# Kernel tuning notes

Hardware: AMD Instinct MI355X
Metric: run time of the kernel (lower is better)

Reference implementation:

```python
import jax, jax.numpy as jnp
import numpy as np

B, S, D, H, E, KW = 2, 2048, 1024, 8, 128, 16  # batch, seq, d_model, heads, head_width, kernel_width


def setup_inputs() -> dict:
    key = jax.random.key(0)
    ks = jax.random.split(key, 10)
    sc = D ** -0.5
    x = jax.random.normal(ks[0], (B, S, D), dtype=jnp.float32)
    Wq = jax.random.normal(ks[1], (H, D, E), dtype=jnp.float32) * sc
    bq = jnp.zeros((H, E), dtype=jnp.float32)
    Wk = jax.random.normal(ks[2], (H, D, E), dtype=jnp.float32) * sc
    bk = jnp.zeros((H, E), dtype=jnp.float32)
    Wv = jax.random.normal(ks[3], (H, D, E), dtype=jnp.float32) * sc
    bv = jnp.zeros((H, E), dtype=jnp.float32)
    Wo = jax.random.normal(ks[4], (H, E, D), dtype=jnp.float32) * ((H * E) ** -0.5)
    bo = jnp.zeros((D,), dtype=jnp.float32)
    dilations = jnp.array([1, 1, 2, 2, 4, 4, 8, 8], dtype=jnp.int32)
    return {"x": x, "Wq": Wq, "bq": bq, "Wk": Wk, "bk": bk,
            "Wv": Wv, "bv": bv, "Wo": Wo, "bo": bo, "dilations": dilations}


def _windows(kh, vh, bkh, bvh, d):
    # kh, vh: [B, S, E] projected keys/values for one head; d: dilation (scalar int)
    s = kh.shape[1]
    # center-justified dilated window: positions i + d*j - d*(KW-1)//2
    pos = jnp.arange(s)[:, None] + d * jnp.arange(KW)[None, :] - (d * (KW - 1)) // 2
    valid = (pos >= 0) & (pos < s)            # [S, KW]
    posc = jnp.clip(pos, 0, s - 1)
    # padded positions hold the zero-embedding, whose projection is just the bias
    kw = jnp.where(valid[None, :, :, None], kh[:, posc, :], bkh)  # [B, S, KW, E]
    vw = jnp.where(valid[None, :, :, None], vh[:, posc, :], bvh)
    return kw, vw


def _lcsa(x, Wq, bq, Wk, bk, Wv, bv, Wo, bo, dilations):
    # per-head independent projections (Core.Linear with parallel shape [heads])
    q = jnp.einsum('bsd,hde->bhse', x, Wq) + bq[None, :, None, :]       # [B,H,S,E]
    k_all = jnp.einsum('bsd,hde->bhse', x, Wk) + bk[None, :, None, :]
    v_all = jnp.einsum('bsd,hde->bhse', x, Wv) + bv[None, :, None, :]
    # gather dilated local windows per head (project-then-gather; padded = bias)
    kw, vw = jax.vmap(_windows, in_axes=(1, 1, 0, 0, 0))(k_all, v_all, bk, bv, dilations)
    # kw, vw: [H, B, S, KW, E]
    logits = jnp.einsum('bhse,hbske->bhsk', q, kw)                       # [B,H,S,KW]
    score = jax.nn.softmax(logits, axis=-1)
    # NOTE: original divides by sqrt(d_head) AFTER softmax*value (faithful quirk)
    attn = jnp.einsum('bhsk,hbske->bhse', score, vw) / jnp.sqrt(jnp.asarray(E, x.dtype))
    out = jnp.einsum('bhse,hed->bsd', attn, Wo) + bo                     # dehead merge
    return out


def reference(x, Wq, bq, Wk, bk, Wv, bv, Wo, bo, dilations):
    return _lcsa(x, Wq, bq, Wk, bk, Wv, bv, Wo, bo, dilations)
```

## Files before the change

### kernel.cpp

```cpp
#include <hip/hip_runtime.h>
#include <stdint.h>

#define Bb 2
#define Ss 2048
#define Dd 1024
#define Hh 8
#define Ee 128
#define KWW 16
#define Mm (Bb*Ss)
#define Kk 1024

typedef unsigned short u16;
typedef __attribute__((ext_vector_type(8))) _Float16 f16x8;
typedef __attribute__((ext_vector_type(4))) float f32x4;

__device__ __forceinline__ u16 f2h(float f) {
  union { _Float16 h; u16 u; } v; v.h = (_Float16)f; return v.u;
}
__device__ __forceinline__ float h2f(u16 u) {
  union { u16 u; _Float16 h; } v; v.u = u; return (float)v.h;
}
__device__ __forceinline__ float h2f_lo(uint32_t w) { return h2f((u16)(w & 0xFFFF)); }
__device__ __forceinline__ float h2f_hi(uint32_t w) { return h2f((u16)(w >> 16)); }

__device__ __forceinline__ void gll16(const void* g, void* l) {
  __builtin_amdgcn_global_load_lds((const __attribute__((address_space(1))) void*)g,
                                   (__attribute__((address_space(3))) void*)l, 16, 0, 0);
}

__global__ __launch_bounds__(256) void prep(
    const float* __restrict__ x, const float* __restrict__ Wq,
    const float* __restrict__ Wk, const float* __restrict__ Wv,
    const float* __restrict__ Wo,
    u16* __restrict__ xh, u16* __restrict__ wT, u16* __restrict__ woT) {
  const int bid = blockIdx.x;
  const int tid = threadIdx.x;
  if (bid < 4096) {
    int i = (bid * 256 + tid) * 4;
    float4 f = *(const float4*)(x + i);
    uint64_t pk = (uint64_t)f2h(f.x) | ((uint64_t)f2h(f.y) << 16) |
                  ((uint64_t)f2h(f.z) << 32) | ((uint64_t)f2h(f.w) << 48);
    *(uint64_t*)(xh + i) = pk;
    return;
  }
  __shared__ float tile[32][33];
  const int tx = tid & 31, ty = tid >> 5;
  if (bid < 4096 + 3072) {
    const int idx = bid - 4096;
    const int z = idx >> 7, rem = idx & 127;
    const int h = z & 7;
    const float* W = (z < 8) ? Wq : (z < 16) ? Wk : Wv;
    const float* ib = W + (size_t)h * Dd * Ee;
    u16* ob = wT + (size_t)z * Ee * Kk;
    const int r0 = (rem & 31) * 32, c0 = (rem >> 5) * 32;
    #pragma unroll
    for (int kq = 0; kq < 4; kq++)
      tile[ty + 8*kq][tx] = ib[(size_t)(r0 + ty + 8*kq) * Ee + (c0 + tx)];
    __syncthreads();
    const int k = r0 + tx;
    #pragma unroll
    for (int kq = 0; kq < 4; kq++) {
      const int n = c0 + ty + 8*kq;
      ob[(((size_t)(k >> 3) * 128 + n) << 3) + (k & 7)] = f2h(tile[tx][ty + 8*kq]);
    }
  } else {
    const int idx = bid - (4096 + 3072);
    const int r0 = (idx & 31) * 32, c0 = (idx >> 5) * 32;
    const int C = Dd;
    #pragma unroll
    for (int kq = 0; kq < 4; kq++)
      tile[ty + 8*kq][tx] = Wo[(size_t)(r0 + ty + 8*kq) * C + (c0 + tx)];
    __syncthreads();
    const int k = r0 + tx;
    #pragma unroll
    for (int kq = 0; kq < 4; kq++) {
      const int n = c0 + ty + 8*kq;
      woT[(size_t)(n >> 7) * 131072 +
          (((size_t)(k >> 3) * 128 + (n & 127)) << 3) + (k & 7)] = f2h(tile[tx][ty + 8*kq]);
    }
  }
}

template<int MT>
__device__ __forceinline__ void gemm_core(
    const u16* __restrict__ A, const u16* __restrict__ Btf,
    u16* As, f32x4 (&acc)[MT / 32][4]) {
  constexpr int MI = MT / 32;
  const int tid = threadIdx.x;
  const int wave = tid >> 6;
  const int lane = tid & 63;
  const size_t lnoff = (size_t)(lane >> 3) * Kk + (size_t)(((lane & 7) ^ (lane >> 3)) * 8);

  const int wm = (wave >> 1) * (MT / 2);
  const int wn = (wave & 1) * 64;
  const int fr = lane & 15;
  const int q  = lane >> 4;
  const int sw = fr & 7;

  const u16* bptr = Btf + ((size_t)q * 128 + wn + fr) * 8;
  f16x8 bcur[8], bnxt[8];
  #pragma unroll
  for (int ks = 0; ks < 2; ks++)
    #pragma unroll
    for (int j = 0; j < 4; j++)
      bcur[ks * 4 + j] = *(const f16x8*)(bptr + (ks * 4) * 1024 + j * 128);

  #pragma unroll
  for (int i = 0; i < MI; i++)
    #pragma unroll
    for (int j = 0; j < 4; j++)
      #pragma unroll
      for (int r = 0; r < 4; r++) acc[i][j][r] = 0.0f;

  #pragma unroll
  for (int c = 0; c < MI; c++)
    gll16(A + lnoff + (size_t)((c * 4 + wave) * 8) * Kk, As + (c * 4 + wave) * 512);
  __syncthreads();

  for (int w = 0; w < Kk / 64; w++) {
    const int kt = w * 64;
    u16* cur = As + (w & 1) * (MT * 64);
    u16* nxt = As + ((w + 1) & 1) * (MT * 64);
    if (w + 1 < Kk / 64) {
      #pragma unroll
      for (int c = 0; c < MI; c++)
        gll16(A + lnoff + (size_t)((c * 4 + wave) * 8) * Kk + kt + 64, nxt + (c * 4 + wave) * 512);
    }
    const int ktn = (kt + 64) & (Kk - 1);
    #pragma unroll
    for (int ks = 0; ks < 2; ks++)
      #pragma unroll
      for (int j = 0; j < 4; j++)
        bnxt[ks * 4 + j] = *(const f16x8*)(bptr + ((ktn >> 3) + ks * 4) * 1024 + j * 128);
    #pragma unroll
    for (int ks = 0; ks < 2; ks++) {
      const int col = ((ks << 2) | q) ^ sw;
      f16x8 ah[MI];
      #pragma unroll
      for (int i = 0; i < MI; i++)
        ah[i] = *(const f16x8*)(cur + (wm + i * 16 + fr) * 64 + col * 8);
      #pragma unroll
      for (int i = 0; i < MI; i++)
        #pragma unroll
        for (int j = 0; j < 4; j++)
          acc[i][j] = __builtin_amdgcn_mfma_f32_16x16x32_f16(ah[i], bcur[ks * 4 + j], acc[i][j], 0, 0, 0);
    }
    __syncthreads();
    #pragma unroll
    for (int t = 0; t < 8; t++) bcur[t] = bnxt[t];
  }
}


__global__ __launch_bounds__(256) void gemm_qkv(
    const u16* __restrict__ xh, const u16* __restrict__ wT,
    const float* __restrict__ bq, const float* __restrict__ bk, const float* __restrict__ bv,
    u16* __restrict__ q, u16* __restrict__ k, u16* __restrict__ v) {
  __shared__ u16 As[128 * 64 * 2];
  const int m0 = blockIdx.x * 128;
  const int z = blockIdx.z;
  const int proj = z >> 3, h = z & 7;
  f32x4 acc[4][4];
  gemm_core<128>(xh + (size_t)m0 * Kk, wT + (size_t)z * (Ee * Kk), As, acc);

  u16* dst = proj == 0 ? q : (proj == 1 ? k : v);
  const float* bias = proj == 0 ? bq : (proj == 1 ? bk : bv);
  const int wave = threadIdx.x >> 6, lane = threadIdx.x & 63;
  const int wm = (wave >> 1) * 64, wn = (wave & 1) * 64;
  const int cn = lane & 15, rq4 = (lane >> 4) * 4;
  #pragma unroll
  for (int j = 0; j < 4; j++) {
    const int e = wn + j * 16 + cn;
    const float bb = bias[h * Ee + e];
    #pragma unroll
    for (int i = 0; i < 4; i++) {
      #pragma unroll
      for (int r = 0; r < 4; r++) {
        const int m = m0 + wm + i * 16 + rq4 + r;
        const int b = m >> 11, s = m & (Ss - 1);
        dst[(((size_t)(b * Hh + h)) * Ss + s) * Ee + e] = f2h(acc[i][j][r] + bb);
      }
    }
  }
}

__global__ __launch_bounds__(256) void gemm_out(
    const u16* __restrict__ attn, const u16* __restrict__ woT,
    const float* __restrict__ bo, float* __restrict__ out) {
  __shared__ u16 As[64 * 64 * 2];
  const int m0 = blockIdx.x * 64;
  const int n0 = blockIdx.y * 128;
  f32x4 acc[2][4];
  gemm_core<64>(attn + (size_t)m0 * Kk, woT + (size_t)blockIdx.y * 131072, As, acc);
  const int wave = threadIdx.x >> 6, lane = threadIdx.x & 63;
  const int wm = (wave >> 1) * 32, wn = (wave & 1) * 64;
  const int cn = lane & 15, rq4 = (lane >> 4) * 4;
  #pragma unroll
  for (int j = 0; j < 4; j++) {
    const int n = n0 + wn + j * 16 + cn;
    const float bb = bo[n];
    #pragma unroll
    for (int i = 0; i < 2; i++) {
      #pragma unroll
      for (int r = 0; r < 4; r++) {
        const int m = m0 + wm + i * 16 + rq4 + r;
        out[(size_t)m * Dd + n] = acc[i][j][r] + bb;
      }
    }
  }
}

__global__ __launch_bounds__(256) void attn_kernel(
    const u16* __restrict__ q, const u16* __restrict__ k, const u16* __restrict__ v,
    const float* __restrict__ bk, const float* __restrict__ bv,
    const int* __restrict__ dil, u16* __restrict__ attn) {
  const int nblk = (Bb * Hh * Ss) / 4;
  const int blk = (blockIdx.x & 7) * (nblk / 8) + (blockIdx.x >> 3);
  const int wid = blk * 4 + (threadIdx.x >> 6);
  const int lane = threadIdx.x & 63;
  const int s = wid & (Ss - 1);
  const int bh = wid >> 11;
  const int h = bh & 7, b = bh >> 3;
  const int d = dil[h];
  const size_t base = (size_t)bh * Ss * Ee;
  const u16* kp = k + base;
  const u16* vp = v + base;
  const uint32_t qw = *(const uint32_t*)(q + base + (size_t)s * Ee + 2 * lane);
  const float qx = h2f_lo(qw), qy = h2f_hi(qw);
  const float2 bk2 = ((const float2*)(bk + h * Ee))[lane];
  const float2 bv2 = ((const float2*)(bv + h * Ee))[lane];
  const int off = (d * (KWW - 1)) >> 1;
  const int J = (lane >> 2) & 15;

  float logit[KWW];
  #pragma unroll
  for (int j = 0; j < KWW; j++) {
    const int pos = s + d * j - off;
    if (pos >= 0 && pos < Ss) {
      uint32_t kw = *(const uint32_t*)(kp + (size_t)pos * Ee + 2 * lane);
      logit[j] = qx * h2f_lo(kw) + qy * h2f_hi(kw);
    } else {
      logit[j] = qx * bk2.x + qy * bk2.y;
    }
  }
  float vvx[KWW], vvy[KWW];
  #pragma unroll
  for (int t = 0; t < KWW; t++) {
    const int j = J ^ t;
    const int pos = s + d * j - off;
    const int posc = min(max(pos, 0), Ss - 1);
    uint32_t vw = *(const uint32_t*)(vp + (size_t)posc * Ee + 2 * lane);
    const bool ok = (pos >= 0) && (pos < Ss);
    vvx[t] = ok ? h2f_lo(vw) : bv2.x;
    vvy[t] = ok ? h2f_hi(vw) : bv2.y;
  }

  {
    const bool hi = (lane & 32) != 0;
    #pragma unroll
    for (int j = 0; j < 8; j++) {
      float send = hi ? logit[j] : logit[j + 8];
      float recv = __shfl_xor(send, 32, 64);
      logit[j] = (hi ? logit[j + 8] : logit[j]) + recv;
    }
  }
  {
    const bool hi = (lane & 16) != 0;
    #pragma unroll
    for (int j = 0; j < 4; j++) {
      float send = hi ? logit[j] : logit[j + 4];
      float recv = __shfl_xor(send, 16, 64);
      logit[j] = (hi ? logit[j + 4] : logit[j]) + recv;
    }
  }
  {
    const bool hi = (lane & 8) != 0;
    #pragma unroll
    for (int j = 0; j < 2; j++) {
      float send = hi ? logit[j] : logit[j + 2];
      float recv = __shfl_xor(send, 8, 64);
      logit[j] = (hi ? logit[j + 2] : logit[j]) + recv;
    }
  }
  float own;
  {
    const bool hi = (lane & 4) != 0;
    float send = hi ? logit[0] : logit[1];
    float recv = __shfl_xor(send, 4, 64);
    own = (hi ? logit[1] : logit[0]) + recv;
  }
  own += __shfl_xor(own, 2, 64);
  own += __shfl_xor(own, 1, 64);

  float mx = own;
  mx = fmaxf(mx, __shfl_xor(mx, 4, 64));
  mx = fmaxf(mx, __shfl_xor(mx, 8, 64));
  mx = fmaxf(mx, __shfl_xor(mx, 16, 64));
  mx = fmaxf(mx, __shfl_xor(mx, 32, 64));
  float w = __expf(own - mx);
  float sum = w;
  sum += __shfl_xor(sum, 4, 64);
  sum += __shfl_xor(sum, 8, 64);
  sum += __shfl_xor(sum, 16, 64);
  sum += __shfl_xor(sum, 32, 64);
  w *= 1.0f / (sum * 11.313708498984760f);

  float g[KWW];
  g[0] = w;
  g[1] = __shfl_xor(g[0], 4, 64);
  #pragma unroll
  for (int t = 0; t < 2; t++) g[2 + t] = __shfl_xor(g[t], 8, 64);
  #pragma unroll
  for (int t = 0; t < 4; t++) g[4 + t] = __shfl_xor(g[t], 16, 64);
  #pragma unroll
  for (int t = 0; t < 8; t++) g[8 + t] = __shfl_xor(g[t], 32, 64);

  float ax = 0.f, ay = 0.f;
  #pragma unroll
  for (int t = 0; t < KWW; t++) { ax += g[t] * vvx[t]; ay += g[t] * vvy[t]; }

  u16* op = attn + ((size_t)(b * Ss + s)) * (Hh * Ee) + h * Ee + 2 * lane;
  *(uint32_t*)op = (uint32_t)f2h(ax) | ((uint32_t)f2h(ay) << 16);
}

extern "C" void kernel_launch(void* const* d_in, const int* in_sizes, int n_in,
                              void* d_out, int out_size, void* d_ws, size_t ws_size,
                              hipStream_t stream) {
  (void)in_sizes; (void)n_in; (void)out_size; (void)ws_size;
  const float* x  = (const float*)d_in[0];
  const float* Wq = (const float*)d_in[1];
  const float* bq = (const float*)d_in[2];
  const float* Wk = (const float*)d_in[3];
  const float* bk = (const float*)d_in[4];
  const float* Wv = (const float*)d_in[5];
  const float* bv = (const float*)d_in[6];
  const float* Wo = (const float*)d_in[7];
  const float* bo = (const float*)d_in[8];
  const int* dil  = (const int*)d_in[9];
  float* out = (float*)d_out;

  char* ws = (char*)d_ws;
  u16* xh  = (u16*)ws;  ws += (size_t)Mm * Kk * 2;
  u16* wT  = (u16*)ws;  ws += (size_t)24 * Ee * Kk * 2;
  u16* woT = (u16*)ws;  ws += (size_t)Kk * Dd * 2;
  u16* q = (u16*)ws; ws += (size_t)Bb * Hh * Ss * Ee * 2;
  u16* k = (u16*)ws; ws += (size_t)Bb * Hh * Ss * Ee * 2;
  u16* v = (u16*)ws; ws += (size_t)Bb * Hh * Ss * Ee * 2;
  u16* attn = xh;

  prep<<<8192, 256, 0, stream>>>(x, Wq, Wk, Wv, Wo, xh, wT, woT);
  gemm_qkv<<<dim3(Mm / 128, 1, 24), 256, 0, stream>>>(xh, wT, bq, bk, bv, q, k, v);
  attn_kernel<<<(Bb * Hh * Ss) / 4, 256, 0, stream>>>(q, k, v, bk, bv, dil, attn);
  gemm_out<<<dim3(Mm / 64, Dd / 128), 256, 0, stream>>>(attn, woT, bo, out);
}
```

Before: 169.2 us.

## Map attention queries to 16-lane groups with 128-bit vector loads

The attention kernel now processes four query positions per wavefront, one per 16-lane group, instead of one per wavefront. Each lane handles 8 head elements through uint4 loads of q, k and v, so the butterfly reductions and softmax shuffles span only 16 lanes. Value rows stay packed as fp16 in registers until accumulation. The aim is fewer memory instructions and fewer shuffles per query, at the cost of higher register pressure from 16 uint4 value rows.

```diff
diff --git a/kernel.cpp b/kernel.cpp
--- a/kernel.cpp
+++ b/kernel.cpp
@@ -214,113 +214,158 @@
     const u16* __restrict__ q, const u16* __restrict__ k, const u16* __restrict__ v,
     const float* __restrict__ bk, const float* __restrict__ bv,
     const int* __restrict__ dil, u16* __restrict__ attn) {
-  const int nblk = (Bb * Hh * Ss) / 4;
+  const int nblk = (Bb * Hh * Ss) / 16;
   const int blk = (blockIdx.x & 7) * (nblk / 8) + (blockIdx.x >> 3);
   const int wid = blk * 4 + (threadIdx.x >> 6);
   const int lane = threadIdx.x & 63;
-  const int s = wid & (Ss - 1);
-  const int bh = wid >> 11;
+  const int grp = lane >> 4;
+  const int lx = lane & 15;
+  const int idx = wid * 4 + grp;
+  const int s = idx & (Ss - 1);
+  const int bh = idx >> 11;
   const int h = bh & 7, b = bh >> 3;
   const int d = dil[h];
   const size_t base = (size_t)bh * Ss * Ee;
   const u16* kp = k + base;
   const u16* vp = v + base;
-  const uint32_t qw = *(const uint32_t*)(q + base + (size_t)s * Ee + 2 * lane);
-  const float qx = h2f_lo(qw), qy = h2f_hi(qw);
-  const float2 bk2 = ((const float2*)(bk + h * Ee))[lane];
-  const float2 bv2 = ((const float2*)(bv + h * Ee))[lane];
+  const int e0 = lx * 8;
   const int off = (d * (KWW - 1)) >> 1;
-  const int J = (lane >> 2) & 15;
+
+  float qf[8];
+  {
+    uint4 qw = *(const uint4*)(q + base + (size_t)s * Ee + e0);
+    qf[0] = h2f_lo(qw.x); qf[1] = h2f_hi(qw.x);
+    qf[2] = h2f_lo(qw.y); qf[3] = h2f_hi(qw.y);
+    qf[4] = h2f_lo(qw.z); qf[5] = h2f_hi(qw.z);
+    qf[6] = h2f_lo(qw.w); qf[7] = h2f_hi(qw.w);
+  }
+  float bkf[8], bvf[8];
+  {
+    const float4 a0 = ((const float4*)(bk + h * Ee + e0))[0];
+    const float4 a1 = ((const float4*)(bk + h * Ee + e0))[1];
+    bkf[0]=a0.x; bkf[1]=a0.y; bkf[2]=a0.z; bkf[3]=a0.w;
+    bkf[4]=a1.x; bkf[5]=a1.y; bkf[6]=a1.z; bkf[7]=a1.w;
+    const float4 c0 = ((const float4*)(bv + h * Ee + e0))[0];
+    const float4 c1 = ((const float4*)(bv + h * Ee + e0))[1];
+    bvf[0]=c0.x; bvf[1]=c0.y; bvf[2]=c0.z; bvf[3]=c0.w;
+    bvf[4]=c1.x; bvf[5]=c1.y; bvf[6]=c1.z; bvf[7]=c1.w;
+  }
+  float blog = 0.f;
+  #pragma unroll
+  for (int i = 0; i < 8; i++) blog += qf[i] * bkf[i];
+  uint4 bvh;
+  bvh.x = (uint32_t)f2h(bvf[0]) | ((uint32_t)f2h(bvf[1]) << 16);
+  bvh.y = (uint32_t)f2h(bvf[2]) | ((uint32_t)f2h(bvf[3]) << 16);
+  bvh.z = (uint32_t)f2h(bvf[4]) | ((uint32_t)f2h(bvf[5]) << 16);
+  bvh.w = (uint32_t)f2h(bvf[6]) | ((uint32_t)f2h(bvf[7]) << 16);
 
   float logit[KWW];
   #pragma unroll
   for (int j = 0; j < KWW; j++) {
     const int pos = s + d * j - off;
-    if (pos >= 0 && pos < Ss) {
-      uint32_t kw = *(const uint32_t*)(kp + (size_t)pos * Ee + 2 * lane);
-      logit[j] = qx * h2f_lo(kw) + qy * h2f_hi(kw);
-    } else {
-      logit[j] = qx * bk2.x + qy * bk2.y;
-    }
-  }
-  float vvx[KWW], vvy[KWW];
+    const int posc = min(max(pos, 0), Ss - 1);
+    uint4 kw = *(const uint4*)(kp + (size_t)posc * Ee + e0);
+    float t = qf[0] * h2f_lo(kw.x) + qf[1] * h2f_hi(kw.x)
+            + qf[2] * h2f_lo(kw.y) + qf[3] * h2f_hi(kw.y)
+            + qf[4] * h2f_lo(kw.z) + qf[5] * h2f_hi(kw.z)
+            + qf[6] * h2f_lo(kw.w) + qf[7] * h2f_hi(kw.w);
+    logit[j] = (pos >= 0 && pos < Ss) ? t : blog;
+  }
+
+  uint4 vrow[KWW];
   #pragma unroll
   for (int t = 0; t < KWW; t++) {
-    const int j = J ^ t;
+    const int j = lx ^ t;
     const int pos = s + d * j - off;
     const int posc = min(max(pos, 0), Ss - 1);
-    uint32_t vw = *(const uint32_t*)(vp + (size_t)posc * Ee + 2 * lane);
+    uint4 vw = *(const uint4*)(vp + (size_t)posc * Ee + e0);
     const bool ok = (pos >= 0) && (pos < Ss);
-    vvx[t] = ok ? h2f_lo(vw) : bv2.x;
-    vvy[t] = ok ? h2f_hi(vw) : bv2.y;
-  }
-
-  {
-    const bool hi = (lane & 32) != 0;
-    #pragma unroll
-    for (int j = 0; j < 8; j++) {
-      float send = hi ? logit[j] : logit[j + 8];
-      float recv = __shfl_xor(send, 32, 64);
-      logit[j] = (hi ? logit[j + 8] : logit[j]) + recv;
-    }
-  }
-  {
-    const bool hi = (lane & 16) != 0;
-    #pragma unroll
-    for (int j = 0; j < 4; j++) {
-      float send = hi ? logit[j] : logit[j + 4];
-      float recv = __shfl_xor(send, 16, 64);
-      logit[j] = (hi ? logit[j + 4] : logit[j]) + recv;
-    }
-  }
-  {
-    const bool hi = (lane & 8) != 0;
-    #pragma unroll
-    for (int j = 0; j < 2; j++) {
-      float send = hi ? logit[j] : logit[j + 2];
+    vrow[t].x = ok ? vw.x : bvh.x;
+    vrow[t].y = ok ? vw.y : bvh.y;
+    vrow[t].z = ok ? vw.z : bvh.z;
+    vrow[t].w = ok ? vw.w : bvh.w;
+  }
+
+  {
+    const bool hi = (lx & 8) != 0;
+    #pragma unroll
+    for (int jj = 0; jj < 8; jj++) {
+      float send = hi ? logit[jj] : logit[jj + 8];
       float recv = __shfl_xor(send, 8, 64);
-      logit[j] = (hi ? logit[j + 2] : logit[j]) + recv;
+      logit[jj] = (hi ? logit[jj + 8] : logit[jj]) + recv;
+    }
+  }
+  {
+    const bool hi = (lx & 4) != 0;
+    #pragma unroll
+    for (int jj = 0; jj < 4; jj++) {
+      float send = hi ? logit[jj] : logit[jj + 4];
+      float recv = __shfl_xor(send, 4, 64);
+      logit[jj] = (hi ? logit[jj + 4] : logit[jj]) + recv;
+    }
+  }
+  {
+    const bool hi = (lx & 2) != 0;
+    #pragma unroll
+    for (int jj = 0; jj < 2; jj++) {
+      float send = hi ? logit[jj] : logit[jj + 2];
+      float recv = __shfl_xor(send, 2, 64);
+      logit[jj] = (hi ? logit[jj + 2] : logit[jj]) + recv;
     }
   }
   float own;
   {
-    const bool hi = (lane & 4) != 0;
+    const bool hi = (lx & 1) != 0;
     float send = hi ? logit[0] : logit[1];
-    float recv = __shfl_xor(send, 4, 64);
+    float recv = __shfl_xor(send, 1, 64);
     own = (hi ? logit[1] : logit[0]) + recv;
   }
-  own += __shfl_xor(own, 2, 64);
-  own += __shfl_xor(own, 1, 64);
 
   float mx = own;
+  mx = fmaxf(mx, __shfl_xor(mx, 1, 64));
+  mx = fmaxf(mx, __shfl_xor(mx, 2, 64));
   mx = fmaxf(mx, __shfl_xor(mx, 4, 64));
   mx = fmaxf(mx, __shfl_xor(mx, 8, 64));
-  mx = fmaxf(mx, __shfl_xor(mx, 16, 64));
-  mx = fmaxf(mx, __shfl_xor(mx, 32, 64));
   float w = __expf(own - mx);
   float sum = w;
+  sum += __shfl_xor(sum, 1, 64);
+  sum += __shfl_xor(sum, 2, 64);
   sum += __shfl_xor(sum, 4, 64);
   sum += __shfl_xor(sum, 8, 64);
-  sum += __shfl_xor(sum, 16, 64);
-  sum += __shfl_xor(sum, 32, 64);
   w *= 1.0f / (sum * 11.313708498984760f);
 
   float g[KWW];
   g[0] = w;
-  g[1] = __shfl_xor(g[0], 4, 64);
-  #pragma unroll
-  for (int t = 0; t < 2; t++) g[2 + t] = __shfl_xor(g[t], 8, 64);
-  #pragma unroll
-  for (int t = 0; t < 4; t++) g[4 + t] = __shfl_xor(g[t], 16, 64);
-  #pragma unroll
-  for (int t = 0; t < 8; t++) g[8 + t] = __shfl_xor(g[t], 32, 64);
-
-  float ax = 0.f, ay = 0.f;
-  #pragma unroll
-  for (int t = 0; t < KWW; t++) { ax += g[t] * vvx[t]; ay += g[t] * vvy[t]; }
-
-  u16* op = attn + ((size_t)(b * Ss + s)) * (Hh * Ee) + h * Ee + 2 * lane;
-  *(uint32_t*)op = (uint32_t)f2h(ax) | ((uint32_t)f2h(ay) << 16);
+  g[1] = __shfl_xor(g[0], 1, 64);
+  #pragma unroll
+  for (int t = 0; t < 2; t++) g[2 + t] = __shfl_xor(g[t], 2, 64);
+  #pragma unroll
+  for (int t = 0; t < 4; t++) g[4 + t] = __shfl_xor(g[t], 4, 64);
+  #pragma unroll
+  for (int t = 0; t < 8; t++) g[8 + t] = __shfl_xor(g[t], 8, 64);
+
+  float acc[8];
+  #pragma unroll
+  for (int i = 0; i < 8; i++) acc[i] = 0.f;
+  #pragma unroll
+  for (int t = 0; t < KWW; t++) {
+    const float wt = g[t];
+    acc[0] += wt * h2f_lo(vrow[t].x);
+    acc[1] += wt * h2f_hi(vrow[t].x);
+    acc[2] += wt * h2f_lo(vrow[t].y);
+    acc[3] += wt * h2f_hi(vrow[t].y);
+    acc[4] += wt * h2f_lo(vrow[t].z);
+    acc[5] += wt * h2f_hi(vrow[t].z);
+    acc[6] += wt * h2f_lo(vrow[t].w);
+    acc[7] += wt * h2f_hi(vrow[t].w);
+  }
+
+  uint4 o;
+  o.x = (uint32_t)f2h(acc[0]) | ((uint32_t)f2h(acc[1]) << 16);
+  o.y = (uint32_t)f2h(acc[2]) | ((uint32_t)f2h(acc[3]) << 16);
+  o.z = (uint32_t)f2h(acc[4]) | ((uint32_t)f2h(acc[5]) << 16);
+  o.w = (uint32_t)f2h(acc[6]) | ((uint32_t)f2h(acc[7]) << 16);
+  *(uint4*)(attn + (size_t)(b * Ss + s) * (Hh * Ee) + h * Ee + e0) = o;
 }
 
 extern "C" void kernel_launch(void* const* d_in, const int* in_sizes, int n_in,
@@ -350,6 +395,6 @@
 
   prep<<<8192, 256, 0, stream>>>(x, Wq, Wk, Wv, Wo, xh, wT, woT);
   gemm_qkv<<<dim3(Mm / 128, 1, 24), 256, 0, stream>>>(xh, wT, bq, bk, bv, q, k, v);
-  attn_kernel<<<(Bb * Hh * Ss) / 4, 256, 0, stream>>>(q, k, v, bk, bv, dil, attn);
+  attn_kernel<<<(Bb * Hh * Ss) / 16, 256, 0, stream>>>(q, k, v, bk, bv, dil, attn);
   gemm_out<<<dim3(Mm / 64, Dd / 128), 256, 0, stream>>>(attn, woT, bo, out);
 }
```

Measured after the change: 158.5 us. 1.07x faster.
